# Optimization experiments

Hardware: AMD Instinct MI355X
Metric: run time of the kernel (lower is better)

## Reference

```python
import jax, jax.numpy as jnp
import numpy as np

NOISE_VAR = 0.001  # std of directional noise (torch Normal(0, noise_var) uses scale)
EPS_NORM = 1e-12
EPS_LOG = 1e-10


def setup_inputs() -> dict:
    key = jax.random.key(0)
    k1, k2, k3 = jax.random.split(key, 3)
    N, D, K = 32768, 256, 8192
    z = jax.random.normal(k1, (N, D), dtype=jnp.float32)
    # torch init: uniform * (1/num_embeddings)
    codebook = jax.random.uniform(k2, (K, D), dtype=jnp.float32) * (1.0 / K)
    noise = jax.random.normal(k3, (N, D), dtype=jnp.float32)
    return {"z": z, "codebook": codebook, "noise": noise}


def reference(z, codebook, noise):
    K = codebook.shape[0]
    # squared L2 distances via ||z||^2 + ||c||^2 - 2 z c^T   -> [N, K]
    distances = (jnp.sum(z * z, axis=1, keepdims=True)
                 + jnp.sum(codebook * codebook, axis=1)
                 - 2.0 * (z @ codebook.T))
    indices = jnp.argmin(distances, axis=1)              # [N]
    z_hard = codebook[indices]                           # [N, D] gather
    direction = z_hard - z
    random_vectors = noise * NOISE_VAR + direction
    norm_rv = jnp.linalg.norm(random_vectors, axis=1, keepdims=True)
    normalized = random_vectors / jnp.maximum(norm_rv, EPS_NORM)
    error_magnitude = jnp.linalg.norm(direction, axis=1, keepdims=True)
    vq_error = error_magnitude * jax.lax.stop_gradient(normalized)
    z_q = z + vq_error
    # perplexity
    counts = jnp.bincount(indices, length=K)
    avg_probs = counts.astype(jnp.float32) / indices.shape[0]
    perplexity = jnp.exp(-jnp.sum(avg_probs * jnp.log(avg_probs + EPS_LOG)))
    return z_q, indices, perplexity
```

## Files before the change

### kernel.cpp

```cpp
#include <hip/hip_runtime.h>
#include <math.h>

#define N_ROWS 32768
#define K_CODES 8192
#define D_DIM 256
#define GUARD 5.0e-5f
#define GUARD_STEPS 4u

typedef unsigned short u16;
typedef unsigned int u32;
typedef float f32x4 __attribute__((ext_vector_type(4)));
typedef short short8 __attribute__((ext_vector_type(8)));

#define GL_LDS(g, l) __builtin_amdgcn_global_load_lds( \
    (const __attribute__((address_space(1))) void*)(g), \
    (__attribute__((address_space(3))) void*)(l), 16, 0, 0)

__device__ __forceinline__ void bf16_split(float x, u16& h, u16& l) {
    unsigned u = __float_as_uint(x);
    unsigned r = (u + 0x7fffu + ((u >> 16) & 1u)) >> 16;
    h = (u16)r;
    float hf = __uint_as_float(r << 16);
    float res = x - hf;
    unsigned u2 = __float_as_uint(res);
    unsigned r2 = (u2 + 0x7fffu + ((u2 >> 16) & 1u)) >> 16;
    l = (u16)r2;
}

__global__ void split_norm_kernel(const float* __restrict__ x, u16* __restrict__ hi,
                                  u16* __restrict__ lo, float* __restrict__ nrm, int nrows) {
    int gid = blockIdx.x * blockDim.x + threadIdx.x;
    int row = gid >> 6;
    int lane = gid & 63;
    if (row >= nrows) return;
    float4 v = ((const float4*)(x + (size_t)row * D_DIM))[lane];
    ushort4 h, l;
    bf16_split(v.x, h.x, l.x);
    bf16_split(v.y, h.y, l.y);
    bf16_split(v.z, h.z, l.z);
    bf16_split(v.w, h.w, l.w);
    ((ushort4*)(hi + (size_t)row * D_DIM))[lane] = h;
    ((ushort4*)(lo + (size_t)row * D_DIM))[lane] = l;
    double s = (double)v.x * v.x + (double)v.y * v.y + (double)v.z * v.z + (double)v.w * v.w;
    #pragma unroll
    for (int off = 32; off; off >>= 1) s += __shfl_xor(s, off);
    if (lane == 0) nrm[row] = (float)s;
}

__global__ void row_norms_kernel(const float* __restrict__ x, float* __restrict__ nrm, int nrows) {
    int gid = blockIdx.x * blockDim.x + threadIdx.x;
    int row = gid >> 6;
    int lane = gid & 63;
    if (row >= nrows) return;
    float4 v = ((const float4*)(x + (size_t)row * D_DIM))[lane];
    double s = (double)v.x * v.x + (double)v.y * v.y + (double)v.z * v.z + (double)v.w * v.w;
    #pragma unroll
    for (int off = 32; off; off >>= 1) s += __shfl_xor(s, off);
    if (lane == 0) nrm[row] = (float)s;
}

__global__ __launch_bounds__(512, 2) void mfma_pass_kernel(
    const u16* __restrict__ z1, const u16* __restrict__ z2,
    const u16* __restrict__ c1, const u16* __restrict__ c2,
    const float* __restrict__ rowN,
    int* __restrict__ idx_i, float* __restrict__ idx_f, int* __restrict__ cand2,
    int* __restrict__ flag_list, int* __restrict__ flag_count)
{
    __shared__ __align__(16) u16 z1s[128 * 256];
    __shared__ __align__(16) u16 z2s[2 * 4 * 128 * 8];
    __shared__ __align__(16) u16 c1s[2 * 4 * 256 * 8];
    __shared__ __align__(16) u16 c2s[2 * 4 * 256 * 8];
    __shared__ u32 mk1[4][128];
    __shared__ u32 mk2[4][128];

    const int tid = threadIdx.x;
    const int lane = tid & 63;
    const int w = tid >> 6;
    const int wm = w >> 2, wn = w & 3;
    const int l15 = lane & 15, l4 = lane >> 4;
    const int row0 = blockIdx.x * 128;

    #pragma unroll
    for (int r = 0; r < 8; ++r) {
        int g = tid + 512 * r;
        int rw = g >> 5, c16 = g & 31;
        GL_LDS(z1 + (size_t)(row0 + rw) * D_DIM + ((c16 ^ (rw & 7)) * 8), z1s + g * 8);
    }

    auto stage = [&](int step, int buf) {
        int ct = step >> 3, kc = step & 7;
        int cb = ct * 256;
        {
            int c16 = tid >> 7, rw = tid & 127;
            GL_LDS(z2 + (size_t)(row0 + rw) * D_DIM + kc * 32 + c16 * 8,
                   z2s + (buf * 512 + tid) * 8);
        }
        #pragma unroll
        for (int r = 0; r < 2; ++r) {
            int g = tid + 512 * r;
            int c16 = g >> 8, cr = g & 255;
            GL_LDS(c1 + (size_t)(cb + cr) * D_DIM + kc * 32 + c16 * 8,
                   c1s + (buf * 1024 + g) * 8);
        }
        #pragma unroll
        for (int r = 0; r < 2; ++r) {
            int g = tid + 512 * r;
            int c16 = g >> 8, cr = g & 255;
            GL_LDS(c2 + (size_t)(cb + cr) * D_DIM + kc * 32 + c16 * 8,
                   c2s + (buf * 1024 + g) * 8);
        }
    };

    float rnv[16];
    u32 rnb[16];
    #pragma unroll
    for (int fm = 0; fm < 4; ++fm)
        #pragma unroll
        for (int r = 0; r < 4; ++r) {
            float rv = rowN[row0 + wm * 64 + fm * 16 + l4 * 4 + r];
            rnv[fm * 4 + r] = rv;
            rnb[fm * 4 + r] = __float_as_uint(rv) - 1024u;
        }

    u32 b1k[16], b2k[16];
    #pragma unroll
    for (int k = 0; k < 16; ++k) { b1k[k] = 0xFFFFFFFFu; b2k[k] = 0xFFFFFFFFu; }

    f32x4 acc[4][4];
    #pragma unroll
    for (int fm = 0; fm < 4; ++fm)
        #pragma unroll
        for (int fn = 0; fn < 4; ++fn) acc[fm][fn] = (f32x4){0.f, 0.f, 0.f, 0.f};

    stage(0, 0);

    for (int step = 0; step < 256; ++step) {
        const int kc = step & 7, buf = step & 1;
        if (step < 255) {
            stage(step + 1, buf ^ 1);
            asm volatile("s_waitcnt vmcnt(5)");
        } else {
            asm volatile("s_waitcnt vmcnt(0)");
        }
        __builtin_amdgcn_s_barrier();

        short8 a1[4], a2[4], b1f[4], b2f[4];
        #pragma unroll
        for (int fm = 0; fm < 4; ++fm) {
            int r = wm * 64 + fm * 16 + l15;
            int c16 = kc * 4 + l4;
            a1[fm] = *(const short8*)(z1s + (r * 32 + (c16 ^ (r & 7))) * 8);
            a2[fm] = *(const short8*)(z2s + (buf * 512 + l4 * 128 + r) * 8);
        }
        #pragma unroll
        for (int fn = 0; fn < 4; ++fn) {
            int cr = wn * 64 + fn * 16 + l15;
            b1f[fn] = *(const short8*)(c1s + (buf * 1024 + l4 * 256 + cr) * 8);
            b2f[fn] = *(const short8*)(c2s + (buf * 1024 + l4 * 256 + cr) * 8);
        }
        #pragma unroll
        for (int fm = 0; fm < 4; ++fm)
            #pragma unroll
            for (int fn = 0; fn < 4; ++fn) {
                acc[fm][fn] = __builtin_amdgcn_mfma_f32_16x16x32_bf16(a1[fm], b1f[fn], acc[fm][fn], 0, 0, 0);
                acc[fm][fn] = __builtin_amdgcn_mfma_f32_16x16x32_bf16(a2[fm], b1f[fn], acc[fm][fn], 0, 0, 0);
                acc[fm][fn] = __builtin_amdgcn_mfma_f32_16x16x32_bf16(a1[fm], b2f[fn], acc[fm][fn], 0, 0, 0);
            }

        if (kc == 7) {
            int cbase = (step >> 3) * 256;
            #pragma unroll
            for (int fn = 0; fn < 4; ++fn) {
                u32 code = (u32)(cbase + wn * 64 + fn * 16 + l15);
                #pragma unroll
                for (int fm = 0; fm < 4; ++fm)
                    #pragma unroll
                    for (int r2 = 0; r2 < 4; ++r2) {
                        int k16 = fm * 4 + r2;
                        float dist = fmaf(-2.0f, acc[fm][fn][r2], rnv[k16]);
                        u32 key = ((__float_as_uint(dist) - rnb[k16]) << 13) + code;
                        u32 t  = b1k[k16] > key ? b1k[k16] : key;
                        b1k[k16] = b1k[k16] < key ? b1k[k16] : key;
                        b2k[k16] = b2k[k16] < t ? b2k[k16] : t;
                        acc[fm][fn][r2] = 0.f;
                    }
            }
        }
        asm volatile("s_waitcnt lgkmcnt(0)");
        __builtin_amdgcn_s_barrier();
    }

    #pragma unroll
    for (int off = 1; off < 16; off <<= 1) {
        #pragma unroll
        for (int k = 0; k < 16; ++k) {
            u32 o1 = (u32)__shfl_xor((int)b1k[k], off);
            u32 o2 = (u32)__shfl_xor((int)b2k[k], off);
            u32 mx = b1k[k] > o1 ? b1k[k] : o1;
            b1k[k] = b1k[k] < o1 ? b1k[k] : o1;
            u32 mn2 = b2k[k] < o2 ? b2k[k] : o2;
            b2k[k] = mn2 < mx ? mn2 : mx;
        }
    }
    if (l15 == 0) {
        #pragma unroll
        for (int fm = 0; fm < 4; ++fm)
            #pragma unroll
            for (int r2 = 0; r2 < 4; ++r2) {
                int rl = wm * 64 + fm * 16 + l4 * 4 + r2;
                mk1[wn][rl] = b1k[fm * 4 + r2];
                mk2[wn][rl] = b2k[fm * 4 + r2];
            }
    }
    __syncthreads();
    if (tid < 128) {
        u32 B1 = 0xFFFFFFFFu, B2 = 0xFFFFFFFFu;
        #pragma unroll
        for (int s = 0; s < 4; ++s) {
            u32 o1 = mk1[s][tid];
            u32 o2 = mk2[s][tid];
            u32 mx = B1 > o1 ? B1 : o1;
            B1 = B1 < o1 ? B1 : o1;
            u32 mn2 = B2 < o2 ? B2 : o2;
            B2 = mn2 < mx ? mn2 : mx;
        }
        int row = row0 + tid;
        int i1 = (int)(B1 & 8191u);
        idx_i[row] = i1;
        idx_f[row] = (float)i1;
        cand2[row] = (int)(B2 & 8191u);
        if ((B2 >> 13) - (B1 >> 13) <= GUARD_STEPS) {
            int p = atomicAdd(flag_count, 1);
            flag_list[p] = row;
        }
    }
}

__global__ __launch_bounds__(256) void lite_rescan_kernel(
    const float* __restrict__ z, const float* __restrict__ cb,
    const float* __restrict__ rowN, const int* __restrict__ flag_list,
    const int* __restrict__ flag_count, const int* __restrict__ cand2,
    int* __restrict__ idx_i, float* __restrict__ idx_f)
{
    int nflag = *flag_count;
    int widx = blockIdx.x * 4 + (threadIdx.x >> 6);
    if (widx >= nflag) return;
    int lane = threadIdx.x & 63;
    int row = flag_list[widx];
    int i1 = idx_i[row];
    int i2 = cand2[row];
    float rn = rowN[row];
    float4 zv = *(const float4*)(z + (size_t)row * D_DIM + lane * 4);
    float4 c1v = *(const float4*)(cb + (size_t)i1 * D_DIM + lane * 4);
    float4 c2v = *(const float4*)(cb + (size_t)i2 * D_DIM + lane * 4);
    float s1 = zv.x * c1v.x;
    s1 = fmaf(zv.y, c1v.y, s1);
    s1 = fmaf(zv.z, c1v.z, s1);
    s1 = fmaf(zv.w, c1v.w, s1);
    float s2 = zv.x * c2v.x;
    s2 = fmaf(zv.y, c2v.y, s2);
    s2 = fmaf(zv.z, c2v.z, s2);
    s2 = fmaf(zv.w, c2v.w, s2);
    #pragma unroll
    for (int off = 32; off; off >>= 1) {
        s1 += __shfl_xor(s1, off);
        s2 += __shfl_xor(s2, off);
    }
    float d1 = fmaf(-2.0f, s1, rn);
    float d2 = fmaf(-2.0f, s2, rn);
    bool w2 = (d2 < d1) || (d2 == d1 && i2 < i1);
    int win = w2 ? i2 : i1;
    if (lane == 0) {
        idx_i[row] = win;
        idx_f[row] = (float)win;
    }
}

__global__ void finalize_kernel(const float* __restrict__ z, const float* __restrict__ cb,
                                const float* __restrict__ noise, const int* __restrict__ idx,
                                float* __restrict__ zq)
{
    int gid = blockIdx.x * blockDim.x + threadIdx.x;
    int row = gid >> 6;
    int lane = gid & 63;
    if (row >= N_ROWS) return;
    const float4* zr = (const float4*)(z + (size_t)row * D_DIM);
    const float4* nr = (const float4*)(noise + (size_t)row * D_DIM);
    int k = idx[row];
    const float4* cr = (const float4*)(cb + (size_t)k * D_DIM);
    float4 zv = zr[lane], nv = nr[lane], cv = cr[lane];
    float4 dir, rv;
    dir.x = cv.x - zv.x; dir.y = cv.y - zv.y; dir.z = cv.z - zv.z; dir.w = cv.w - zv.w;
    rv.x = nv.x * 0.001f + dir.x; rv.y = nv.y * 0.001f + dir.y;
    rv.z = nv.z * 0.001f + dir.z; rv.w = nv.w * 0.001f + dir.w;
    float s_d = dir.x*dir.x + dir.y*dir.y + dir.z*dir.z + dir.w*dir.w;
    float s_r = rv.x*rv.x + rv.y*rv.y + rv.z*rv.z + rv.w*rv.w;
    #pragma unroll
    for (int off = 32; off; off >>= 1) {
        s_d += __shfl_xor(s_d, off);
        s_r += __shfl_xor(s_r, off);
    }
    float mag = sqrtf(s_d);
    float nrm = sqrtf(s_r);
    float scale = mag / fmaxf(nrm, 1e-12f);
    float4 o;
    o.x = zv.x + rv.x * scale; o.y = zv.y + rv.y * scale;
    o.z = zv.z + rv.z * scale; o.w = zv.w + rv.w * scale;
    ((float4*)(zq + (size_t)row * D_DIM))[lane] = o;
}

__global__ void zero_kernel(int* __restrict__ h, int* __restrict__ cnt) {
    int i = blockIdx.x * 256 + threadIdx.x;
    if (i < K_CODES) h[i] = 0;
    if (i == K_CODES) *cnt = 0;
}
__global__ void hist_kernel(const int* __restrict__ idx, int* __restrict__ h) {
    int i = blockIdx.x * blockDim.x + threadIdx.x;
    if (i < N_ROWS) atomicAdd(&h[idx[i]], 1);
}
__global__ void perplexity_kernel(const int* __restrict__ h, float* __restrict__ out) {
    __shared__ double red[256];
    int tid = threadIdx.x;
    double s = 0.0;
    for (int j = tid; j < K_CODES; j += 256) {
        float p = (float)h[j] / 32768.0f;
        float t = p * logf(p + 1e-10f);
        s += (double)t;
    }
    red[tid] = s;
    __syncthreads();
    for (int off = 128; off; off >>= 1) {
        if (tid < off) red[tid] += red[tid + off];
        __syncthreads();
    }
    if (tid == 0) out[0] = (float)exp(-red[0]);
}

#define BM 64
#define BN 128
#define BD 32
#define TM 4
#define TN 8
__global__ __launch_bounds__(256) void argmin_kernel(
    const float* __restrict__ z, const float* __restrict__ cb,
    const float* __restrict__ rowN, const float* __restrict__ codeN,
    int* __restrict__ idx_out, float* __restrict__ idx_f_out)
{
    __shared__ float As[BD][BM + 4];
    __shared__ float Bs[BD][BN + 4];
    const int tid = threadIdx.x;
    const int tx = tid & 15;
    const int ty = tid >> 4;
    const int row0 = blockIdx.x * BM;
    float rn[TM];
    #pragma unroll
    for (int tm = 0; tm < TM; ++tm) rn[tm] = rowN[row0 + ty * TM + tm];
    float bestVal[TM]; int bestIdx[TM];
    #pragma unroll
    for (int tm = 0; tm < TM; ++tm) { bestVal[tm] = INFINITY; bestIdx[tm] = 0; }
    for (int t0 = 0; t0 < K_CODES; t0 += BN) {
        float acc[TM][TN];
        #pragma unroll
        for (int tm = 0; tm < TM; ++tm)
            #pragma unroll
            for (int tn = 0; tn < TN; ++tn) acc[tm][tn] = 0.0f;
        for (int d0 = 0; d0 < D_DIM; d0 += BD) {
            __syncthreads();
            #pragma unroll
            for (int r = 0; r < 2; ++r) {
                int g = tid + 256 * r;
                int m = g >> 3, seg = g & 7;
                float4 v = *(const float4*)(z + (size_t)(row0 + m) * D_DIM + d0 + seg * 4);
                As[seg * 4 + 0][m] = v.x; As[seg * 4 + 1][m] = v.y;
                As[seg * 4 + 2][m] = v.z; As[seg * 4 + 3][m] = v.w;
            }
            #pragma unroll
            for (int r = 0; r < 4; ++r) {
                int g = tid + 256 * r;
                int c = g >> 3, seg = g & 7;
                float4 v = *(const float4*)(cb + (size_t)(t0 + c) * D_DIM + d0 + seg * 4);
                Bs[seg * 4 + 0][c] = v.x; Bs[seg * 4 + 1][c] = v.y;
                Bs[seg * 4 + 2][c] = v.z; Bs[seg * 4 + 3][c] = v.w;
            }
            __syncthreads();
            #pragma unroll
            for (int d = 0; d < BD; ++d) {
                float a[TM], b[TN];
                #pragma unroll
                for (int tm = 0; tm < TM; ++tm) a[tm] = As[d][ty * TM + tm];
                #pragma unroll
                for (int tn = 0; tn < TN; ++tn) b[tn] = Bs[d][tx * TN + tn];
                #pragma unroll
                for (int tm = 0; tm < TM; ++tm)
                    #pragma unroll
                    for (int tn = 0; tn < TN; ++tn)
                        acc[tm][tn] = fmaf(a[tm], b[tn], acc[tm][tn]);
            }
        }
        #pragma unroll
        for (int tn = 0; tn < TN; ++tn) {
            int code = t0 + tx * TN + tn;
            float cn = codeN[code];
            #pragma unroll
            for (int tm = 0; tm < TM; ++tm) {
                float c2 = 2.0f * acc[tm][tn];
                float ts = rn[tm] + cn;
                float dist = ts - c2;
                if (dist < bestVal[tm]) { bestVal[tm] = dist; bestIdx[tm] = code; }
            }
        }
    }
    #pragma unroll
    for (int off = 8; off; off >>= 1) {
        #pragma unroll
        for (int tm = 0; tm < TM; ++tm) {
            float ov = __shfl_xor(bestVal[tm], off, 16);
            int   oi = __shfl_xor(bestIdx[tm], off, 16);
            if (ov < bestVal[tm] || (ov == bestVal[tm] && oi < bestIdx[tm])) {
                bestVal[tm] = ov; bestIdx[tm] = oi;
            }
        }
    }
    if (tx == 0) {
        #pragma unroll
        for (int tm = 0; tm < TM; ++tm) {
            int row = row0 + ty * TM + tm;
            idx_out[row] = bestIdx[tm];
            idx_f_out[row] = (float)bestIdx[tm];
        }
    }
}

extern "C" void kernel_launch(void* const* d_in, const int* in_sizes, int n_in,
                              void* d_out, int out_size, void* d_ws, size_t ws_size,
                              hipStream_t stream)
{
    const float* z     = (const float*)d_in[0];
    const float* cb    = (const float*)d_in[1];
    const float* noise = (const float*)d_in[2];

    float* out   = (float*)d_out;
    float* zq    = out;
    float* idx_f = out + (size_t)N_ROWS * D_DIM;
    float* perp  = idx_f + N_ROWS;

    char* ws = (char*)d_ws;

    const size_t OFF_Z1    = 0;
    const size_t OFF_Z2    = 16777216;
    const size_t OFF_C1    = 33554432;
    const size_t OFF_C2    = 37748736;
    const size_t OFF_ROWN  = 41943040;
    const size_t OFF_CODN  = 42074112;
    const size_t OFF_IDX   = 42106880;
    const size_t OFF_FLAGL = 42237952;
    const size_t OFF_FLAGC = 42369024;
    const size_t OFF_HIST  = 42369280;
    const size_t OFF_CAND2 = 42402048;
    const size_t NEED      = 42533120;

    if (ws_size >= NEED) {
        u16*   z1    = (u16*)(ws + OFF_Z1);
        u16*   z2    = (u16*)(ws + OFF_Z2);
        u16*   c1    = (u16*)(ws + OFF_C1);
        u16*   c2    = (u16*)(ws + OFF_C2);
        float* rowN  = (float*)(ws + OFF_ROWN);
        int*   idxi  = (int*)(ws + OFF_IDX);
        int*   flagl = (int*)(ws + OFF_FLAGL);
        int*   flagc = (int*)(ws + OFF_FLAGC);
        int*   hist  = (int*)(ws + OFF_HIST);
        int*   cand2 = (int*)(ws + OFF_CAND2);

        split_norm_kernel<<<N_ROWS / 4, 256, 0, stream>>>(z, z1, z2, rowN, N_ROWS);
        split_norm_kernel<<<K_CODES / 4, 256, 0, stream>>>(cb, c1, c2, (float*)(ws + OFF_CODN), K_CODES);
        zero_kernel<<<33, 256, 0, stream>>>(hist, flagc);
        mfma_pass_kernel<<<N_ROWS / 128, 512, 0, stream>>>(z1, z2, c1, c2, rowN,
                                                           idxi, idx_f, cand2, flagl, flagc);
        lite_rescan_kernel<<<N_ROWS / 4, 256, 0, stream>>>(z, cb, rowN, flagl, flagc,
                                                           cand2, idxi, idx_f);
        hist_kernel<<<N_ROWS / 256, 256, 0, stream>>>(idxi, hist);
        finalize_kernel<<<(N_ROWS * 64) / 256, 256, 0, stream>>>(z, cb, noise, idxi, zq);
        perplexity_kernel<<<1, 256, 0, stream>>>(hist, perp);
    } else {
        int*   idxi  = (int*)ws;
        int*   hist  = (int*)(ws + (size_t)N_ROWS * 4);
        float* rowN  = (float*)(ws + (size_t)(N_ROWS + K_CODES) * 4);
        float* codeN = (float*)(ws + (size_t)(2 * N_ROWS + K_CODES) * 4);
        int*   fc    = (int*)(ws + (size_t)(2 * N_ROWS + 2 * K_CODES) * 4);

        row_norms_kernel<<<N_ROWS / 4, 256, 0, stream>>>(z, rowN, N_ROWS);
        row_norms_kernel<<<K_CODES / 4, 256, 0, stream>>>(cb, codeN, K_CODES);
        argmin_kernel<<<N_ROWS / BM, 256, 0, stream>>>(z, cb, rowN, codeN, idxi, idx_f);
        zero_kernel<<<33, 256, 0, stream>>>(hist, fc);
        hist_kernel<<<N_ROWS / 256, 256, 0, stream>>>(idxi, hist);
        finalize_kernel<<<(N_ROWS * 64) / 256, 256, 0, stream>>>(z, cb, noise, idxi, zq);
        perplexity_kernel<<<1, 256, 0, stream>>>(hist, perp);
    }
}
```

Before: 663.1 us.

## Shrink MFMA distance tile to 64 rows with single-buffered 64-wide K chunks

```diff
diff --git a/kernel.cpp b/kernel.cpp
--- a/kernel.cpp
+++ b/kernel.cpp
@@ -4,7 +4,6 @@
 #define N_ROWS 32768
 #define K_CODES 8192
 #define D_DIM 256
-#define GUARD 5.0e-5f
 #define GUARD_STEPS 4u
 
 typedef unsigned short u16;
@@ -59,57 +58,23 @@
     if (lane == 0) nrm[row] = (float)s;
 }
 
-__global__ __launch_bounds__(512, 2) void mfma_pass_kernel(
+__global__ __launch_bounds__(256, 2) void mfma_pass_kernel(
     const u16* __restrict__ z1, const u16* __restrict__ z2,
     const u16* __restrict__ c1, const u16* __restrict__ c2,
     const float* __restrict__ rowN,
     int* __restrict__ idx_i, float* __restrict__ idx_f, int* __restrict__ cand2,
     int* __restrict__ flag_list, int* __restrict__ flag_count)
 {
-    __shared__ __align__(16) u16 z1s[128 * 256];
-    __shared__ __align__(16) u16 z2s[2 * 4 * 128 * 8];
-    __shared__ __align__(16) u16 c1s[2 * 4 * 256 * 8];
-    __shared__ __align__(16) u16 c2s[2 * 4 * 256 * 8];
-    __shared__ u32 mk1[4][128];
-    __shared__ u32 mk2[4][128];
+    __shared__ __align__(16) u16 z1s[8 * 64 * 8];
+    __shared__ __align__(16) u16 z2s[8 * 64 * 8];
+    __shared__ __align__(16) u16 c1s[8 * 256 * 8];
+    __shared__ __align__(16) u16 c2s[8 * 256 * 8];
 
     const int tid = threadIdx.x;
     const int lane = tid & 63;
-    const int w = tid >> 6;
-    const int wm = w >> 2, wn = w & 3;
+    const int wn = tid >> 6;
     const int l15 = lane & 15, l4 = lane >> 4;
-    const int row0 = blockIdx.x * 128;
-
-    #pragma unroll
-    for (int r = 0; r < 8; ++r) {
-        int g = tid + 512 * r;
-        int rw = g >> 5, c16 = g & 31;
-        GL_LDS(z1 + (size_t)(row0 + rw) * D_DIM + ((c16 ^ (rw & 7)) * 8), z1s + g * 8);
-    }
-
-    auto stage = [&](int step, int buf) {
-        int ct = step >> 3, kc = step & 7;
-        int cb = ct * 256;
-        {
-            int c16 = tid >> 7, rw = tid & 127;
-            GL_LDS(z2 + (size_t)(row0 + rw) * D_DIM + kc * 32 + c16 * 8,
-                   z2s + (buf * 512 + tid) * 8);
-        }
-        #pragma unroll
-        for (int r = 0; r < 2; ++r) {
-            int g = tid + 512 * r;
-            int c16 = g >> 8, cr = g & 255;
-            GL_LDS(c1 + (size_t)(cb + cr) * D_DIM + kc * 32 + c16 * 8,
-                   c1s + (buf * 1024 + g) * 8);
-        }
-        #pragma unroll
-        for (int r = 0; r < 2; ++r) {
-            int g = tid + 512 * r;
-            int c16 = g >> 8, cr = g & 255;
-            GL_LDS(c2 + (size_t)(cb + cr) * D_DIM + kc * 32 + c16 * 8,
-                   c2s + (buf * 1024 + g) * 8);
-        }
-    };
+    const int row0 = blockIdx.x * 64;
 
     float rnv[16];
     u32 rnb[16];
@@ -117,7 +82,7 @@
     for (int fm = 0; fm < 4; ++fm)
         #pragma unroll
         for (int r = 0; r < 4; ++r) {
-            float rv = rowN[row0 + wm * 64 + fm * 16 + l4 * 4 + r];
+            float rv = rowN[row0 + fm * 16 + l4 * 4 + r];
             rnv[fm * 4 + r] = rv;
             rnb[fm * 4 + r] = __float_as_uint(rv) - 1024u;
         }
@@ -132,62 +97,79 @@
         #pragma unroll
         for (int fn = 0; fn < 4; ++fn) acc[fm][fn] = (f32x4){0.f, 0.f, 0.f, 0.f};
 
-    stage(0, 0);
-
-    for (int step = 0; step < 256; ++step) {
-        const int kc = step & 7, buf = step & 1;
-        if (step < 255) {
-            stage(step + 1, buf ^ 1);
-            asm volatile("s_waitcnt vmcnt(5)");
-        } else {
-            asm volatile("s_waitcnt vmcnt(0)");
-        }
-        __builtin_amdgcn_s_barrier();
-
-        short8 a1[4], a2[4], b1f[4], b2f[4];
-        #pragma unroll
-        for (int fm = 0; fm < 4; ++fm) {
-            int r = wm * 64 + fm * 16 + l15;
-            int c16 = kc * 4 + l4;
-            a1[fm] = *(const short8*)(z1s + (r * 32 + (c16 ^ (r & 7))) * 8);
-            a2[fm] = *(const short8*)(z2s + (buf * 512 + l4 * 128 + r) * 8);
-        }
-        #pragma unroll
-        for (int fn = 0; fn < 4; ++fn) {
-            int cr = wn * 64 + fn * 16 + l15;
-            b1f[fn] = *(const short8*)(c1s + (buf * 1024 + l4 * 256 + cr) * 8);
-            b2f[fn] = *(const short8*)(c2s + (buf * 1024 + l4 * 256 + cr) * 8);
-        }
-        #pragma unroll
-        for (int fm = 0; fm < 4; ++fm)
-            #pragma unroll
-            for (int fn = 0; fn < 4; ++fn) {
-                acc[fm][fn] = __builtin_amdgcn_mfma_f32_16x16x32_bf16(a1[fm], b1f[fn], acc[fm][fn], 0, 0, 0);
-                acc[fm][fn] = __builtin_amdgcn_mfma_f32_16x16x32_bf16(a2[fm], b1f[fn], acc[fm][fn], 0, 0, 0);
-                acc[fm][fn] = __builtin_amdgcn_mfma_f32_16x16x32_bf16(a1[fm], b2f[fn], acc[fm][fn], 0, 0, 0);
-            }
-
-        if (kc == 7) {
-            int cbase = (step >> 3) * 256;
-            #pragma unroll
-            for (int fn = 0; fn < 4; ++fn) {
-                u32 code = (u32)(cbase + wn * 64 + fn * 16 + l15);
+    for (int ct = 0; ct < 32; ++ct) {
+        const int cbase = ct * 256;
+        for (int kc = 0; kc < 4; ++kc) {
+            const int ko = kc * 64;
+            __syncthreads();
+            #pragma unroll
+            for (int r = 0; r < 2; ++r) {
+                int s = tid + 256 * r;
+                int seg = s >> 6, rw = s & 63;
+                GL_LDS(z1 + (size_t)(row0 + rw) * D_DIM + ko + seg * 8, z1s + s * 8);
+            }
+            #pragma unroll
+            for (int r = 0; r < 2; ++r) {
+                int s = tid + 256 * r;
+                int seg = s >> 6, rw = s & 63;
+                GL_LDS(z2 + (size_t)(row0 + rw) * D_DIM + ko + seg * 8, z2s + s * 8);
+            }
+            #pragma unroll
+            for (int r = 0; r < 8; ++r) {
+                int s = tid + 256 * r;
+                int seg = s >> 8, cr = s & 255;
+                GL_LDS(c1 + (size_t)(cbase + cr) * D_DIM + ko + seg * 8, c1s + s * 8);
+            }
+            #pragma unroll
+            for (int r = 0; r < 8; ++r) {
+                int s = tid + 256 * r;
+                int seg = s >> 8, cr = s & 255;
+                GL_LDS(c2 + (size_t)(cbase + cr) * D_DIM + ko + seg * 8, c2s + s * 8);
+            }
+            __syncthreads();
+
+            #pragma unroll
+            for (int kk = 0; kk < 2; ++kk) {
+                const int seg = kk * 4 + l4;
+                short8 a1[4], a2[4], b1f[4], b2f[4];
+                #pragma unroll
+                for (int fm = 0; fm < 4; ++fm) {
+                    int rw = fm * 16 + l15;
+                    a1[fm] = *(const short8*)(z1s + (seg * 64 + rw) * 8);
+                    a2[fm] = *(const short8*)(z2s + (seg * 64 + rw) * 8);
+                }
+                #pragma unroll
+                for (int fn = 0; fn < 4; ++fn) {
+                    int cr = wn * 64 + fn * 16 + l15;
+                    b1f[fn] = *(const short8*)(c1s + (seg * 256 + cr) * 8);
+                    b2f[fn] = *(const short8*)(c2s + (seg * 256 + cr) * 8);
+                }
                 #pragma unroll
                 for (int fm = 0; fm < 4; ++fm)
                     #pragma unroll
-                    for (int r2 = 0; r2 < 4; ++r2) {
-                        int k16 = fm * 4 + r2;
-                        float dist = fmaf(-2.0f, acc[fm][fn][r2], rnv[k16]);
-                        u32 key = ((__float_as_uint(dist) - rnb[k16]) << 13) + code;
-                        u32 t  = b1k[k16] > key ? b1k[k16] : key;
-                        b1k[k16] = b1k[k16] < key ? b1k[k16] : key;
-                        b2k[k16] = b2k[k16] < t ? b2k[k16] : t;
-                        acc[fm][fn][r2] = 0.f;
+                    for (int fn = 0; fn < 4; ++fn) {
+                        acc[fm][fn] = __builtin_amdgcn_mfma_f32_16x16x32_bf16(a1[fm], b1f[fn], acc[fm][fn], 0, 0, 0);
+                        acc[fm][fn] = __builtin_amdgcn_mfma_f32_16x16x32_bf16(a2[fm], b1f[fn], acc[fm][fn], 0, 0, 0);
+                        acc[fm][fn] = __builtin_amdgcn_mfma_f32_16x16x32_bf16(a1[fm], b2f[fn], acc[fm][fn], 0, 0, 0);
                     }
             }
         }
-        asm volatile("s_waitcnt lgkmcnt(0)");
-        __builtin_amdgcn_s_barrier();
+        #pragma unroll
+        for (int fn = 0; fn < 4; ++fn) {
+            u32 code = (u32)(cbase + wn * 64 + fn * 16 + l15);
+            #pragma unroll
+            for (int fm = 0; fm < 4; ++fm)
+                #pragma unroll
+                for (int r2 = 0; r2 < 4; ++r2) {
+                    int k16 = fm * 4 + r2;
+                    float dist = fmaf(-2.0f, acc[fm][fn][r2], rnv[k16]);
+                    u32 key = ((__float_as_uint(dist) - rnb[k16]) << 13) + code;
+                    u32 t  = b1k[k16] > key ? b1k[k16] : key;
+                    b1k[k16] = b1k[k16] < key ? b1k[k16] : key;
+                    b2k[k16] = b2k[k16] < t ? b2k[k16] : t;
+                    acc[fm][fn][r2] = 0.f;
+                }
+        }
     }
 
     #pragma unroll
@@ -202,23 +184,26 @@
             b2k[k] = mn2 < mx ? mn2 : mx;
         }
     }
+    __syncthreads();
+    u32* mk1 = (u32*)z1s;
+    u32* mk2 = (u32*)z2s;
     if (l15 == 0) {
         #pragma unroll
         for (int fm = 0; fm < 4; ++fm)
             #pragma unroll
             for (int r2 = 0; r2 < 4; ++r2) {
-                int rl = wm * 64 + fm * 16 + l4 * 4 + r2;
-                mk1[wn][rl] = b1k[fm * 4 + r2];
-                mk2[wn][rl] = b2k[fm * 4 + r2];
+                int rl = fm * 16 + l4 * 4 + r2;
+                mk1[wn * 64 + rl] = b1k[fm * 4 + r2];
+                mk2[wn * 64 + rl] = b2k[fm * 4 + r2];
             }
     }
     __syncthreads();
-    if (tid < 128) {
+    if (tid < 64) {
         u32 B1 = 0xFFFFFFFFu, B2 = 0xFFFFFFFFu;
         #pragma unroll
         for (int s = 0; s < 4; ++s) {
-            u32 o1 = mk1[s][tid];
-            u32 o2 = mk2[s][tid];
+            u32 o1 = mk1[s * 64 + tid];
+            u32 o2 = mk2[s * 64 + tid];
             u32 mx = B1 > o1 ? B1 : o1;
             B1 = B1 < o1 ? B1 : o1;
             u32 mn2 = B2 < o2 ? B2 : o2;
@@ -474,8 +459,8 @@
         split_norm_kernel<<<N_ROWS / 4, 256, 0, stream>>>(z, z1, z2, rowN, N_ROWS);
         split_norm_kernel<<<K_CODES / 4, 256, 0, stream>>>(cb, c1, c2, (float*)(ws + OFF_CODN), K_CODES);
         zero_kernel<<<33, 256, 0, stream>>>(hist, flagc);
-        mfma_pass_kernel<<<N_ROWS / 128, 512, 0, stream>>>(z1, z2, c1, c2, rowN,
-                                                           idxi, idx_f, cand2, flagl, flagc);
+        mfma_pass_kernel<<<N_ROWS / 64, 256, 0, stream>>>(z1, z2, c1, c2, rowN,
+                                                          idxi, idx_f, cand2, flagl, flagc);
         lite_rescan_kernel<<<N_ROWS / 4, 256, 0, stream>>>(z, cb, rowN, flagl, flagc,
                                                            cand2, idxi, idx_f);
         hist_kernel<<<N_ROWS / 256, 256, 0, stream>>>(idxi, hist);
```

Result: slower. 844.3 us (+27.3%).

## Restructure MFMA pass: K-major z1 layout, early LDS wait, setprio, reuse LDS

Applied to the files above, without the earlier changes.

```diff
diff --git a/kernel.cpp b/kernel.cpp
--- a/kernel.cpp
+++ b/kernel.cpp
@@ -4,8 +4,8 @@
 #define N_ROWS 32768
 #define K_CODES 8192
 #define D_DIM 256
-#define GUARD 5.0e-5f
 #define GUARD_STEPS 4u
+#define NCHUNK 256
 
 typedef unsigned short u16;
 typedef unsigned int u32;
@@ -66,12 +66,10 @@
     int* __restrict__ idx_i, float* __restrict__ idx_f, int* __restrict__ cand2,
     int* __restrict__ flag_list, int* __restrict__ flag_count)
 {
-    __shared__ __align__(16) u16 z1s[128 * 256];
-    __shared__ __align__(16) u16 z2s[2 * 4 * 128 * 8];
-    __shared__ __align__(16) u16 c1s[2 * 4 * 256 * 8];
-    __shared__ __align__(16) u16 c2s[2 * 4 * 256 * 8];
-    __shared__ u32 mk1[4][128];
-    __shared__ u32 mk2[4][128];
+    __shared__ __align__(16) u16 z1s[32 * 128 * 8];
+    __shared__ __align__(16) u16 z2s[2][4 * 128 * 8];
+    __shared__ __align__(16) u16 c1s[2][4 * 256 * 8];
+    __shared__ __align__(16) u16 c2s[2][4 * 256 * 8];
 
     const int tid = threadIdx.x;
     const int lane = tid & 63;
@@ -82,32 +80,29 @@
 
     #pragma unroll
     for (int r = 0; r < 8; ++r) {
-        int g = tid + 512 * r;
-        int rw = g >> 5, c16 = g & 31;
-        GL_LDS(z1 + (size_t)(row0 + rw) * D_DIM + ((c16 ^ (rw & 7)) * 8), z1s + g * 8);
-    }
-
-    auto stage = [&](int step, int buf) {
-        int ct = step >> 3, kc = step & 7;
-        int cb = ct * 256;
+        int s = tid + 512 * r;
+        int seg = s >> 7, rw = s & 127;
+        GL_LDS(z1 + (size_t)(row0 + rw) * D_DIM + seg * 8, z1s + s * 8);
+    }
+
+    auto stage_chunk = [&](int c, int buf) {
+        const int ct = c >> 3, kc = c & 7;
+        const int cb = ct * 256, ko = kc * 32;
         {
-            int c16 = tid >> 7, rw = tid & 127;
-            GL_LDS(z2 + (size_t)(row0 + rw) * D_DIM + kc * 32 + c16 * 8,
-                   z2s + (buf * 512 + tid) * 8);
+            int seg = tid >> 7, rw = tid & 127;
+            GL_LDS(z2 + (size_t)(row0 + rw) * D_DIM + ko + seg * 8, z2s[buf] + tid * 8);
         }
         #pragma unroll
         for (int r = 0; r < 2; ++r) {
-            int g = tid + 512 * r;
-            int c16 = g >> 8, cr = g & 255;
-            GL_LDS(c1 + (size_t)(cb + cr) * D_DIM + kc * 32 + c16 * 8,
-                   c1s + (buf * 1024 + g) * 8);
+            int s = tid + 512 * r;
+            int seg = s >> 8, cr = s & 255;
+            GL_LDS(c1 + (size_t)(cb + cr) * D_DIM + ko + seg * 8, c1s[buf] + s * 8);
         }
         #pragma unroll
         for (int r = 0; r < 2; ++r) {
-            int g = tid + 512 * r;
-            int c16 = g >> 8, cr = g & 255;
-            GL_LDS(c2 + (size_t)(cb + cr) * D_DIM + kc * 32 + c16 * 8,
-                   c2s + (buf * 1024 + g) * 8);
+            int s = tid + 512 * r;
+            int seg = s >> 8, cr = s & 255;
+            GL_LDS(c2 + (size_t)(cb + cr) * D_DIM + ko + seg * 8, c2s[buf] + s * 8);
         }
     };
 
@@ -132,32 +127,37 @@
         #pragma unroll
         for (int fn = 0; fn < 4; ++fn) acc[fm][fn] = (f32x4){0.f, 0.f, 0.f, 0.f};
 
-    stage(0, 0);
-
-    for (int step = 0; step < 256; ++step) {
-        const int kc = step & 7, buf = step & 1;
-        if (step < 255) {
-            stage(step + 1, buf ^ 1);
-            asm volatile("s_waitcnt vmcnt(5)");
+    stage_chunk(0, 0);
+
+    for (int c = 0; c < NCHUNK; ++c) {
+        const int buf = c & 1;
+        const int kc = c & 7;
+
+        if (c + 1 < NCHUNK) {
+            stage_chunk(c + 1, buf ^ 1);
+            asm volatile("s_waitcnt vmcnt(5)" ::: "memory");
         } else {
-            asm volatile("s_waitcnt vmcnt(0)");
+            asm volatile("s_waitcnt vmcnt(0)" ::: "memory");
         }
         __builtin_amdgcn_s_barrier();
 
         short8 a1[4], a2[4], b1f[4], b2f[4];
         #pragma unroll
         for (int fm = 0; fm < 4; ++fm) {
-            int r = wm * 64 + fm * 16 + l15;
-            int c16 = kc * 4 + l4;
-            a1[fm] = *(const short8*)(z1s + (r * 32 + (c16 ^ (r & 7))) * 8);
-            a2[fm] = *(const short8*)(z2s + (buf * 512 + l4 * 128 + r) * 8);
+            int rw = wm * 64 + fm * 16 + l15;
+            a1[fm] = *(const short8*)(z1s + ((kc * 4 + l4) * 128 + rw) * 8);
+            a2[fm] = *(const short8*)(z2s[buf] + (l4 * 128 + rw) * 8);
         }
         #pragma unroll
         for (int fn = 0; fn < 4; ++fn) {
             int cr = wn * 64 + fn * 16 + l15;
-            b1f[fn] = *(const short8*)(c1s + (buf * 1024 + l4 * 256 + cr) * 8);
-            b2f[fn] = *(const short8*)(c2s + (buf * 1024 + l4 * 256 + cr) * 8);
-        }
+            b1f[fn] = *(const short8*)(c1s[buf] + (l4 * 256 + cr) * 8);
+            b2f[fn] = *(const short8*)(c2s[buf] + (l4 * 256 + cr) * 8);
+        }
+
+        asm volatile("s_waitcnt lgkmcnt(0)" ::: "memory");
+        __builtin_amdgcn_sched_barrier(0);
+        __builtin_amdgcn_s_setprio(1);
         #pragma unroll
         for (int fm = 0; fm < 4; ++fm)
             #pragma unroll
@@ -166,9 +166,11 @@
                 acc[fm][fn] = __builtin_amdgcn_mfma_f32_16x16x32_bf16(a2[fm], b1f[fn], acc[fm][fn], 0, 0, 0);
                 acc[fm][fn] = __builtin_amdgcn_mfma_f32_16x16x32_bf16(a1[fm], b2f[fn], acc[fm][fn], 0, 0, 0);
             }
+        __builtin_amdgcn_s_setprio(0);
+        __builtin_amdgcn_s_barrier();
 
         if (kc == 7) {
-            int cbase = (step >> 3) * 256;
+            const int cbase = (c >> 3) * 256;
             #pragma unroll
             for (int fn = 0; fn < 4; ++fn) {
                 u32 code = (u32)(cbase + wn * 64 + fn * 16 + l15);
@@ -179,15 +181,13 @@
                         int k16 = fm * 4 + r2;
                         float dist = fmaf(-2.0f, acc[fm][fn][r2], rnv[k16]);
                         u32 key = ((__float_as_uint(dist) - rnb[k16]) << 13) + code;
-                        u32 t  = b1k[k16] > key ? b1k[k16] : key;
+                        u32 mx = b1k[k16] > key ? b1k[k16] : key;
                         b1k[k16] = b1k[k16] < key ? b1k[k16] : key;
-                        b2k[k16] = b2k[k16] < t ? b2k[k16] : t;
+                        b2k[k16] = b2k[k16] < mx ? b2k[k16] : mx;
                         acc[fm][fn][r2] = 0.f;
                     }
             }
         }
-        asm volatile("s_waitcnt lgkmcnt(0)");
-        __builtin_amdgcn_s_barrier();
     }
 
     #pragma unroll
@@ -202,14 +202,17 @@
             b2k[k] = mn2 < mx ? mn2 : mx;
         }
     }
+    __syncthreads();
+    u32* mk1 = (u32*)&z2s[0][0];
+    u32* mk2 = mk1 + 512;
     if (l15 == 0) {
         #pragma unroll
         for (int fm = 0; fm < 4; ++fm)
             #pragma unroll
             for (int r2 = 0; r2 < 4; ++r2) {
                 int rl = wm * 64 + fm * 16 + l4 * 4 + r2;
-                mk1[wn][rl] = b1k[fm * 4 + r2];
-                mk2[wn][rl] = b2k[fm * 4 + r2];
+                mk1[wn * 128 + rl] = b1k[fm * 4 + r2];
+                mk2[wn * 128 + rl] = b2k[fm * 4 + r2];
             }
     }
     __syncthreads();
@@ -217,8 +220,8 @@
         u32 B1 = 0xFFFFFFFFu, B2 = 0xFFFFFFFFu;
         #pragma unroll
         for (int s = 0; s < 4; ++s) {
-            u32 o1 = mk1[s][tid];
-            u32 o2 = mk2[s][tid];
+            u32 o1 = mk1[s * 128 + tid];
+            u32 o2 = mk2[s * 128 + tid];
             u32 mx = B1 > o1 ? B1 : o1;
             B1 = B1 < o1 ? B1 : o1;
             u32 mn2 = B2 < o2 ? B2 : o2;
```

After: 638.7 us. 3.7% less time.
